# Kernel optimization log

Measured on AMD Instinct MI355X. Metric: run time of the kernel, lower is better.

The kernel has to match this reference:

```python
import jax, jax.numpy as jnp
import numpy as np

# Static graph layout: B equal-sized graphs of N nodes, DEG random edges per node.
B, N, DEG = 128, 1024, 16
F_IN, H, C = 2, 64, 2
RATIO = 0.8
E = B * N * DEG
K1 = int(np.ceil(RATIO * N))      # 820
K2 = int(np.ceil(RATIO * K1))     # 656
K3 = int(np.ceil(RATIO * K2))     # 525


def setup_inputs() -> dict:
    key = jax.random.key(0)
    ks = jax.random.split(key, 24)
    x = jax.random.normal(ks[0], (B * N, F_IN), jnp.float32)
    edge_attr = jax.random.uniform(ks[1], (E,), jnp.float32)
    # per-graph random endpoints, offset so edges stay inside each graph
    local = jax.random.randint(ks[2], (2, B, N * DEG), 0, N)
    edge_index = (local + (jnp.arange(B) * N)[None, :, None]).reshape(2, E)

    def lin(k, i, o):
        return jax.random.normal(k, (i, o), jnp.float32) / np.sqrt(i)

    def bias(k, o):
        return jax.random.normal(k, (o,), jnp.float32) * 0.01

    return {
        "x": x, "edge_attr": edge_attr,
        "W1": lin(ks[3], F_IN, H), "b1": bias(ks[4], H),
        "Wp1": lin(ks[5], H, 1), "bp1": bias(ks[6], 1),
        "W2": lin(ks[7], H, H), "b2": bias(ks[8], H),
        "Wp2": lin(ks[9], H, 1), "bp2": bias(ks[10], 1),
        "W3": lin(ks[11], H, H), "b3": bias(ks[12], H),
        "Wp3": lin(ks[13], H, 1), "bp3": bias(ks[14], 1),
        "Wl1": lin(ks[15], 2 * H, H), "bl1": bias(ks[16], H),
        "Wl2": lin(ks[17], H, H // 2), "bl2": bias(ks[18], H // 2),
        "Wl3": lin(ks[19], H // 2, C), "bl3": bias(ks[20], C),
        "edge_index": edge_index,
    }


def gcn(x, src, dst, w, W, b):
    """PyG GCNConv with gcn_norm (self-loops weight 1)."""
    h = x @ W                                       # [BN, out]
    deg = jnp.zeros((x.shape[0],), x.dtype).at[dst].add(w) + 1.0
    dinv = jax.lax.rsqrt(deg)
    norm = dinv[src] * w * dinv[dst]                # [E]
    out = jnp.zeros_like(h).at[dst].add(norm[:, None] * h[src])
    out = out + (dinv * dinv)[:, None] * h          # self-loop term
    return out + b


def sagpool(x, alive, src, dst, Wp, bp, k):
    """SAGPool: unweighted GCN scoring, per-graph top-k, x <- x * tanh(score).
    Removed nodes/edges are kept as masked (alive=False) slots -> static shapes."""
    we = (alive[src] & alive[dst]).astype(x.dtype)
    score = gcn(x, src, dst, we, Wp, bp)[:, 0]      # [BN]
    s = jnp.where(alive, score, -jnp.inf).reshape(B, N)
    _, idx = jax.lax.top_k(s, k)                    # [B, k]
    alive_new = jnp.zeros((B, N), bool).at[jnp.arange(B)[:, None], idx].set(True).reshape(-1)
    xn = jnp.where(alive_new[:, None], x * jnp.tanh(score)[:, None], 0.0)
    return xn, alive_new


def readout(x, alive):
    """concat(global_max_pool, global_mean_pool) over alive nodes per graph."""
    xr = x.reshape(B, N, -1)
    m = alive.reshape(B, N, 1)
    mx = jnp.max(jnp.where(m, xr, -jnp.inf), axis=1)
    mn = jnp.sum(jnp.where(m, xr, 0.0), axis=1) / jnp.sum(m, axis=1).astype(x.dtype)
    return jnp.concatenate([mx, mn], axis=1)        # [B, 2*H]


def _forward(x, edge_attr, W1, b1, Wp1, bp1, W2, b2, Wp2, bp2, W3, b3, Wp3, bp3,
             Wl1, bl1, Wl2, bl2, Wl3, bl3, edge_index):
    src, dst = edge_index[0], edge_index[1]
    h = jax.nn.relu(gcn(x, src, dst, edge_attr, W1, b1))
    h, a1 = sagpool(h, jnp.ones((B * N,), bool), src, dst, Wp1, bp1, K1)
    x1 = readout(h, a1)

    ea1 = edge_attr * (a1[src] & a1[dst]).astype(x.dtype)
    h = jax.nn.relu(gcn(h, src, dst, ea1, W2, b2))
    h, a2 = sagpool(h, a1, src, dst, Wp2, bp2, K2)
    x2 = readout(h, a2)

    # conv3 is called WITHOUT edge_weight -> surviving edges get weight 1
    ea2 = (a2[src] & a2[dst]).astype(x.dtype)
    h = jax.nn.relu(gcn(h, src, dst, ea2, W3, b3))
    h, a3 = sagpool(h, a2, src, dst, Wp3, bp3, K3)
    x3 = readout(h, a3)

    g = x1 + x2 + x3
    g = jax.nn.relu(g @ Wl1 + bl1)                  # dropout: eval mode (identity)
    g = jax.nn.relu(g @ Wl2 + bl2)
    return jax.nn.log_softmax(g @ Wl3 + bl3, axis=-1)


def reference(x, edge_attr, W1, b1, Wp1, bp1, W2, b2, Wp2, bp2, W3, b3, Wp3, bp3,
              Wl1, bl1, Wl2, bl2, Wl3, bl3, edge_index):
    return _forward(x, edge_attr, W1, b1, Wp1, bp1, W2, b2, Wp2, bp2, W3, b3,
                    Wp3, bp3, Wl1, bl1, Wl2, bl2, Wl3, bl3, edge_index)
```

## Files before the change

kernel.cpp:

```cpp
#include <hip/hip_runtime.h>
#include <math.h>

#define NB 128
#define NN 1024
#define BNODES (NB*NN)
#define NE 2097152
#define EPG (NE/NB)
#define EPT (EPG/NN)
#define FH 64
#define KK1 820
#define KK2 656
#define KK3 525

__global__ __launch_bounds__(1024) void k_csr(const int* __restrict__ ei,
                                              const float* __restrict__ ea,
                                              int* __restrict__ rowptr,
                                              int2* __restrict__ csr_sw,
                                              float* __restrict__ dinvW,
                                              float* __restrict__ dinvU) {
  extern __shared__ int2 lcsr[];
  __shared__ int cnt[NN];
  __shared__ int cur[NN];
  __shared__ float wsum[NN];
  int b = blockIdx.x, t = threadIdx.x;
  int node = b*NN + t;
  cnt[t] = 0;
  wsum[t] = 0.f;
  __syncthreads();
  int ebase = b*EPG;
  int se[EPT]; int de[EPT]; float we[EPT];
  #pragma unroll
  for (int i = 0; i < EPT; ++i) {
    int e = ebase + i*NN + t;
    se[i] = ei[e];
    de[i] = ei[NE + e] - b*NN;
    we[i] = ea[e];
    atomicAdd(&cnt[de[i]], 1);
    atomicAdd(&wsum[de[i]], we[i]);
  }
  __syncthreads();
  int v = cnt[t];
  for (int off = 1; off < NN; off <<= 1) {
    int u = (t >= off) ? cnt[t - off] : 0;
    __syncthreads();
    cnt[t] += u;
    __syncthreads();
  }
  int excl = cnt[t] - v;
  rowptr[node] = ebase + excl;
  cur[t] = excl;
  dinvW[node] = rsqrtf(1.f + wsum[t]);
  dinvU[node] = rsqrtf(1.f + (float)v);
  if (b == NB-1 && t == NN-1) rowptr[BNODES] = NE;
  __syncthreads();
  #pragma unroll
  for (int i = 0; i < EPT; ++i) {
    int pos = atomicAdd(&cur[de[i]], 1);
    lcsr[pos] = make_int2(se[i], __float_as_int(we[i]));
  }
  __syncthreads();
  float4* dst4 = (float4*)(csr_sw + ebase);
  const float4* src4 = (const float4*)lcsr;
  #pragma unroll
  for (int i = 0; i < EPG/2/NN; ++i)
    dst4[i*NN + t] = src4[i*NN + t];
}

template<int MODE, bool L1S>
__global__ __launch_bounds__(1024, 4) void k_gath(
    const int* __restrict__ rowptr, const int2* __restrict__ csr_sw,
    const float* __restrict__ dinvW, const float* __restrict__ src,
    const float* __restrict__ Wl,
    const float* __restrict__ bias, const float* __restrict__ Wp,
    float* __restrict__ hA, float* __restrict__ qpart) {
  extern __shared__ float sHB[];
  __shared__ float sDW[NN];
  __shared__ float sWp[32];
  __shared__ float sB[32];
  __shared__ float sW1[64];
  int b = blockIdx.x >> 1, half = blockIdx.x & 1;
  int t = threadIdx.x, l8 = t & 7;
  int gbase = b*NN;
  sDW[t] = dinvW[gbase + t];
  if (t < 32) { sWp[t] = Wp[half*32 + t]; sB[t] = bias[half*32 + t]; }
  float4* sHB4 = (float4*)sHB;
  if (L1S) {
    if (t < 32) { sW1[t] = Wl[half*32 + t]; sW1[32 + t] = Wl[64 + half*32 + t]; }
    __syncthreads();
    #pragma unroll
    for (int i = 0; i < 32; ++i) {
      int el = i*1024 + t;
      int n = el >> 5, ff = el & 31;
      float x0 = src[(size_t)(gbase + n)*2];
      float x1 = src[(size_t)(gbase + n)*2 + 1];
      sHB[n*32 + ff] = x0*sW1[ff] + x1*sW1[32 + ff];
    }
  } else {
    const float4* hB4 = (const float4*)src;
    #pragma unroll
    for (int i = 0; i < 8; ++i) {
      int idx = i*1024 + t;
      int n = idx >> 3, j = idx & 7;
      sHB4[n*8 + j] = hB4[(size_t)(gbase + n)*16 + half*8 + j];
    }
  }
  __syncthreads();
  float4 bv = ((const float4*)sB)[l8];
  float4 wp = ((const float4*)sWp)[l8];
  #pragma unroll 1
  for (int pass = 0; pass < 8; ++pass) {
    int n = pass*128 + (t >> 3);
    int gn = gbase + n;
    float dd = sDW[n];
    float4 hv = sHB4[n*8 + l8];
    float dd2 = dd*dd;
    float4 acc;
    acc.x = fmaf(dd2, hv.x, bv.x);
    acc.y = fmaf(dd2, hv.y, bv.y);
    acc.z = fmaf(dd2, hv.z, bv.z);
    acc.w = fmaf(dd2, hv.w, bv.w);
    int r0 = rowptr[gn], r1 = rowptr[gn+1];
    for (int base = r0; base < r1; base += 8) {
      int sj = 0; float cj = 0.f;
      if (base + l8 < r1) {
        int2 p = csr_sw[base + l8];
        sj = p.x - gbase;
        float w = (MODE == 2) ? 1.f : __int_as_float(p.y);
        cj = sDW[sj] * w * dd;
      }
      float4 v[8];
      #pragma unroll
      for (int j = 0; j < 8; ++j) {
        int s = __shfl(sj, j, 8);
        v[j] = sHB4[s*8 + l8];
      }
      #pragma unroll
      for (int j = 0; j < 8; ++j) {
        float c = __shfl(cj, j, 8);
        acc.x = fmaf(c, v[j].x, acc.x);
        acc.y = fmaf(c, v[j].y, acc.y);
        acc.z = fmaf(c, v[j].z, acc.z);
        acc.w = fmaf(c, v[j].w, acc.w);
      }
    }
    acc.x = fmaxf(acc.x, 0.f); acc.y = fmaxf(acc.y, 0.f);
    acc.z = fmaxf(acc.z, 0.f); acc.w = fmaxf(acc.w, 0.f);
    ((float4*)hA)[(size_t)gn*16 + half*8 + l8] = acc;
    float dot = acc.x*wp.x + acc.y*wp.y + acc.z*wp.z + acc.w*wp.w;
    dot += __shfl_xor(dot, 4, 8);
    dot += __shfl_xor(dot, 2, 8);
    dot += __shfl_xor(dot, 1, 8);
    if (l8 == 0) qpart[half*BNODES + gn] = dot;
  }
}

template<int NEXTMODE>
__global__ __launch_bounds__(1024) void k_pool(
    const int* __restrict__ rowptr, const int2* __restrict__ csr_sw,
    const float* __restrict__ qpart, const float* __restrict__ bp, int k,
    float* __restrict__ tm, int* __restrict__ aliveN,
    float* dinvW, float* dinvU) {
  __shared__ float sq[NN];
  __shared__ float sdU[NN];
  __shared__ float sc[NN];
  __shared__ float sraw[NN];
  __shared__ int ssel[NN];
  int b = blockIdx.x, t = threadIdx.x;
  int gbase = b*NN;
  float du = dinvU[gbase + t];
  sdU[t] = du;
  sq[t] = du * (qpart[gbase + t] + qpart[BNODES + gbase + t]);
  __syncthreads();
  int l16 = t & 15, g = t >> 4;
  float bpv = bp[0];
  for (int i = 0; i < 16; ++i) {
    int n = g*16 + i;
    int gn = gbase + n;
    int r0 = rowptr[gn], r1 = rowptr[gn+1];
    float sum = 0.f;
    for (int base = r0; base < r1; base += 16)
      if (base + l16 < r1) sum += sq[csr_sw[base + l16].x - gbase];
    #pragma unroll
    for (int off = 8; off; off >>= 1) sum += __shfl_xor(sum, off, 16);
    if (l16 == 0) {
      float dun = sdU[n];
      float raw = bpv + dun*(sq[n] + sum);
      sraw[n] = raw;
      sc[n] = (dun != 0.f) ? raw : -INFINITY;
    }
  }
  __syncthreads();
  float me = sc[t];
  int rank = 0;
  const float4* sc4 = (const float4*)sc;
  for (int j4 = 0; j4 < NN/4; ++j4) {
    float4 o = sc4[j4];
    int jb = j4*4;
    rank += (o.x > me) || (o.x == me && jb+0 < t);
    rank += (o.y > me) || (o.y == me && jb+1 < t);
    rank += (o.z > me) || (o.z == me && jb+2 < t);
    rank += (o.w > me) || (o.w == me && jb+3 < t);
  }
  int sel = (rank < k) ? 1 : 0;
  ssel[t] = sel;
  aliveN[gbase + t] = sel;
  tm[gbase + t] = sel ? tanhf(sraw[t]) : 0.f;
  __syncthreads();
  if (NEXTMODE != 0) {
    for (int i = 0; i < 16; ++i) {
      int n = g*16 + i;
      int gn = gbase + n;
      int r0 = rowptr[gn], r1 = rowptr[gn+1];
      float sW = 0.f, sU = 0.f;
      for (int base = r0; base < r1; base += 16)
        if (base + l16 < r1) {
          int2 p = csr_sw[base + l16];
          if (ssel[p.x - gbase]) {
            sW += (NEXTMODE == 2) ? 1.f : __int_as_float(p.y);
            sU += 1.f;
          }
        }
      #pragma unroll
      for (int off = 8; off; off >>= 1) {
        sW += __shfl_xor(sW, off, 16);
        sU += __shfl_xor(sU, off, 16);
      }
      if (l16 == 0) {
        bool dA = ssel[n] != 0;
        dinvW[gn] = dA ? rsqrtf(1.f + sW) : 0.f;
        dinvU[gn] = dA ? rsqrtf(1.f + sU) : 0.f;
      }
    }
  }
}

template<bool DOLIN>
__global__ void k_srl(const float* __restrict__ hA, const float* __restrict__ tm,
                      const int* __restrict__ aliveN, const float* __restrict__ W,
                      float* __restrict__ hB,
                      float* __restrict__ pmax, float* __restrict__ psum) {
  __shared__ float sX[64][65];
  __shared__ float sW[64*64];
  __shared__ int sAl[64];
  __shared__ float rm[4][FH], rs[4][FH];
  int t = threadIdx.x;
  int blk = blockIdx.x;
  int nb = blk*64;
  if (DOLIN)
    for (int i = t; i < 1024; i += 256) ((float4*)sW)[i] = ((const float4*)W)[i];
  if (t < 64) sAl[t] = aliveN[nb + t];
  #pragma unroll
  for (int i = 0; i < 16; ++i) {
    int gidx = (nb << 6) + i*256 + t;
    int node = gidx >> 6, f = gidx & 63;
    sX[node - nb][f] = hA[gidx] * tm[node];
  }
  __syncthreads();
  {
    int f = t & 63, r = t >> 6;
    float mx = -INFINITY, sm = 0.f;
    #pragma unroll
    for (int i = 0; i < 16; ++i) {
      int n = r + i*4;
      float v = sX[n][f];
      if (sAl[n]) { mx = fmaxf(mx, v); sm += v; }
    }
    rm[r][f] = mx; rs[r][f] = sm;
  }
  __syncthreads();
  if (t < FH) {
    float m2 = fmaxf(fmaxf(rm[0][t], rm[1][t]), fmaxf(rm[2][t], rm[3][t]));
    float s2 = rs[0][t] + rs[1][t] + rs[2][t] + rs[3][t];
    pmax[blk*FH + t] = m2;
    psum[blk*FH + t] = s2;
  }
  if (DOLIN) {
    int node = t >> 2;
    int f0 = (t & 3) * 16;
    float4 a0 = {0,0,0,0}, a1 = a0, a2 = a0, a3 = a0;
    #pragma unroll 4
    for (int k = 0; k < 64; ++k) {
      float xv = sX[node][k];
      const float4 w0 = *(const float4*)&sW[k*64 + f0];
      const float4 w1 = *(const float4*)&sW[k*64 + f0 + 4];
      const float4 w2 = *(const float4*)&sW[k*64 + f0 + 8];
      const float4 w3 = *(const float4*)&sW[k*64 + f0 + 12];
      a0.x = fmaf(xv, w0.x, a0.x); a0.y = fmaf(xv, w0.y, a0.y);
      a0.z = fmaf(xv, w0.z, a0.z); a0.w = fmaf(xv, w0.w, a0.w);
      a1.x = fmaf(xv, w1.x, a1.x); a1.y = fmaf(xv, w1.y, a1.y);
      a1.z = fmaf(xv, w1.z, a1.z); a1.w = fmaf(xv, w1.w, a1.w);
      a2.x = fmaf(xv, w2.x, a2.x); a2.y = fmaf(xv, w2.y, a2.y);
      a2.z = fmaf(xv, w2.z, a2.z); a2.w = fmaf(xv, w2.w, a2.w);
      a3.x = fmaf(xv, w3.x, a3.x); a3.y = fmaf(xv, w3.y, a3.y);
      a3.z = fmaf(xv, w3.z, a3.z); a3.w = fmaf(xv, w3.w, a3.w);
    }
    float4* dst = (float4*)(hB + (size_t)(nb + node)*FH + f0);
    dst[0] = a0; dst[1] = a1; dst[2] = a2; dst[3] = a3;
  }
}

__global__ void k_mlp(const float* __restrict__ pmax, const float* __restrict__ psum,
                      const float* __restrict__ Wl1, const float* __restrict__ bl1,
                      const float* __restrict__ Wl2, const float* __restrict__ bl2,
                      const float* __restrict__ Wl3, const float* __restrict__ bl3,
                      float* __restrict__ out) {
  __shared__ float sg[2*FH];
  __shared__ float l1[FH];
  __shared__ float l2[FH/2];
  __shared__ float l3[2];
  int b = blockIdx.x, t = threadIdx.x;
  const float kf[3] = {(float)KK1, (float)KK2, (float)KK3};
  float gm = 0.f, gs = 0.f;
  #pragma unroll
  for (int l = 0; l < 3; ++l) {
    const float* pm = pmax + (size_t)l*NB*16*FH + (b*16)*FH;
    const float* ps = psum + (size_t)l*NB*16*FH + (b*16)*FH;
    float mm = -INFINITY, ss = 0.f;
    #pragma unroll
    for (int p = 0; p < 16; ++p) {
      mm = fmaxf(mm, pm[p*FH + t]);
      ss += ps[p*FH + t];
    }
    gm += mm;
    gs += ss / kf[l];
  }
  sg[t] = gm;
  sg[FH + t] = gs;
  __syncthreads();
  float acc = bl1[t];
  #pragma unroll
  for (int k = 0; k < 2*FH; ++k) acc = fmaf(sg[k], Wl1[k*FH + t], acc);
  l1[t] = fmaxf(acc, 0.f);
  __syncthreads();
  if (t < 32) {
    float a2 = bl2[t];
    #pragma unroll
    for (int k = 0; k < FH; ++k) a2 = fmaf(l1[k], Wl2[k*32 + t], a2);
    l2[t] = fmaxf(a2, 0.f);
  }
  __syncthreads();
  if (t < 2) {
    float a3 = bl3[t];
    #pragma unroll
    for (int k = 0; k < 32; ++k) a3 = fmaf(l2[k], Wl3[k*2 + t], a3);
    l3[t] = a3;
  }
  __syncthreads();
  if (t == 0) {
    float m = fmaxf(l3[0], l3[1]);
    float lse = m + logf(expf(l3[0]-m) + expf(l3[1]-m));
    out[b*2+0] = l3[0] - lse;
    out[b*2+1] = l3[1] - lse;
  }
}

extern "C" void kernel_launch(void* const* d_in, const int* in_sizes, int n_in,
                              void* d_out, int out_size, void* d_ws, size_t ws_size,
                              hipStream_t stream) {
  const float* x   = (const float*)d_in[0];
  const float* ea  = (const float*)d_in[1];
  const float* W1  = (const float*)d_in[2];
  const float* b1  = (const float*)d_in[3];
  const float* Wp1 = (const float*)d_in[4];
  const float* bp1 = (const float*)d_in[5];
  const float* W2  = (const float*)d_in[6];
  const float* b2  = (const float*)d_in[7];
  const float* Wp2 = (const float*)d_in[8];
  const float* bp2 = (const float*)d_in[9];
  const float* W3  = (const float*)d_in[10];
  const float* b3  = (const float*)d_in[11];
  const float* Wp3 = (const float*)d_in[12];
  const float* bp3 = (const float*)d_in[13];
  const float* Wl1 = (const float*)d_in[14];
  const float* bl1 = (const float*)d_in[15];
  const float* Wl2 = (const float*)d_in[16];
  const float* bl2 = (const float*)d_in[17];
  const float* Wl3 = (const float*)d_in[18];
  const float* bl3 = (const float*)d_in[19];
  const int*   ei  = (const int*)d_in[20];
  float* out = (float*)d_out;

  int2* csr_sw = (int2*)d_ws;
  float* hA    = (float*)(csr_sw + NE);
  float* hB    = hA + (size_t)BNODES*FH;
  float* dinvW = hB + (size_t)BNODES*FH;
  float* dinvU = dinvW + BNODES;
  float* qpart = dinvU + BNODES;
  float* tm    = qpart + 2*BNODES;
  float* pmax  = tm + BNODES;
  float* psum  = pmax + 3*NB*16*FH;
  int* aliveN  = (int*)(psum + 3*NB*16*FH);
  int* rowptr  = aliveN + BNODES;

  const size_t gathLds = (size_t)NN*32*sizeof(float);
  const int gS = BNODES/64;

  k_csr<<<NB, 1024, EPG*sizeof(int2), stream>>>(ei, ea, rowptr, csr_sw, dinvW, dinvU);

  k_gath<0,true><<<NB*2, 1024, gathLds, stream>>>(rowptr, csr_sw, dinvW, x, W1, b1, Wp1, hA, qpart);
  k_pool<1><<<NB, 1024, 0, stream>>>(rowptr, csr_sw, qpart, bp1, KK1, tm, aliveN, dinvW, dinvU);
  k_srl<true><<<gS, 256, 0, stream>>>(hA, tm, aliveN, W2, hB, pmax, psum);

  k_gath<1,false><<<NB*2, 1024, gathLds, stream>>>(rowptr, csr_sw, dinvW, hB, W1, b2, Wp2, hA, qpart);
  k_pool<2><<<NB, 1024, 0, stream>>>(rowptr, csr_sw, qpart, bp2, KK2, tm, aliveN, dinvW, dinvU);
  k_srl<true><<<gS, 256, 0, stream>>>(hA, tm, aliveN, W3, hB, pmax + NB*16*FH, psum + NB*16*FH);

  k_gath<2,false><<<NB*2, 1024, gathLds, stream>>>(rowptr, csr_sw, dinvW, hB, W1, b3, Wp3, hA, qpart);
  k_pool<0><<<NB, 1024, 0, stream>>>(rowptr, csr_sw, qpart, bp3, KK3, tm, aliveN, dinvW, dinvU);
  k_srl<false><<<gS, 256, 0, stream>>>(hA, tm, aliveN, W3, hB, pmax + 2*NB*16*FH, psum + 2*NB*16*FH);

  k_mlp<<<NB, FH, 0, stream>>>(pmax, psum, Wl1, bl1, Wl2, bl2, Wl3, bl3, out);
}
```

Baseline: 445.0 us.

## Split per-graph pooling kernel into wider-grid score, top-k, and degree kernels

Replaces the monolithic per-graph k_pool (128 blocks of 1024 threads) with four kernels: q finalisation, neighbor-sum scoring, top-k ranking split four ways per graph, and degree recomputation. The aim is to spread the neighbor gathers and rank counting over far more blocks so the GPU is better occupied, instead of 128 blocks doing serial loops. In exchange it adds more kernel launches and global round trips for q and score that previously stayed in LDS. Degree recomputation now reads alive flags from global memory.

Result: faster. 375.1 us (-15.7%).

```diff
diff --git a/kernel.cpp b/kernel.cpp
--- a/kernel.cpp
+++ b/kernel.cpp
@@ -154,83 +154,86 @@
   }
 }
 
-template<int NEXTMODE>
-__global__ __launch_bounds__(1024) void k_pool(
-    const int* __restrict__ rowptr, const int2* __restrict__ csr_sw,
-    const float* __restrict__ qpart, const float* __restrict__ bp, int k,
-    float* __restrict__ tm, int* __restrict__ aliveN,
-    float* dinvW, float* dinvU) {
-  __shared__ float sq[NN];
-  __shared__ float sdU[NN];
+__global__ void k_qfin(const float* __restrict__ dinvU, const float* __restrict__ qp,
+                       float* __restrict__ q) {
+  int i = blockIdx.x*256 + threadIdx.x;
+  if (i < BNODES) q[i] = dinvU[i]*(qp[i] + qp[BNODES + i]);
+}
+
+__global__ void k_score(const int* __restrict__ rowptr, const int2* __restrict__ csr_sw,
+                        const float* __restrict__ dinvU, const float* __restrict__ q,
+                        const float* __restrict__ bp, float* __restrict__ score) {
+  int t = threadIdx.x;
+  int l16 = t & 15;
+  int d = blockIdx.x*16 + (t >> 4);
+  float du = dinvU[d];
+  float sum = 0.f;
+  if (du != 0.f) {
+    int r0 = rowptr[d], r1 = rowptr[d+1];
+    for (int base = r0; base < r1; base += 16)
+      if (base + l16 < r1) sum += q[csr_sw[base + l16].x];
+  }
+  #pragma unroll
+  for (int off = 8; off; off >>= 1) sum += __shfl_xor(sum, off, 16);
+  if (l16 == 0) score[d] = bp[0] + du*(q[d] + sum);
+}
+
+__global__ void k_topk(const float* __restrict__ score,
+                       const float* __restrict__ dinvU, int k,
+                       float* __restrict__ tm, int* __restrict__ aliveN) {
   __shared__ float sc[NN];
-  __shared__ float sraw[NN];
-  __shared__ int ssel[NN];
-  int b = blockIdx.x, t = threadIdx.x;
+  int b = blockIdx.x >> 2, p = blockIdx.x & 3;
+  int t = threadIdx.x;
   int gbase = b*NN;
-  float du = dinvU[gbase + t];
-  sdU[t] = du;
-  sq[t] = du * (qpart[gbase + t] + qpart[BNODES + gbase + t]);
-  __syncthreads();
-  int l16 = t & 15, g = t >> 4;
-  float bpv = bp[0];
-  for (int i = 0; i < 16; ++i) {
-    int n = g*16 + i;
-    int gn = gbase + n;
-    int r0 = rowptr[gn], r1 = rowptr[gn+1];
-    float sum = 0.f;
-    for (int base = r0; base < r1; base += 16)
-      if (base + l16 < r1) sum += sq[csr_sw[base + l16].x - gbase];
-    #pragma unroll
-    for (int off = 8; off; off >>= 1) sum += __shfl_xor(sum, off, 16);
-    if (l16 == 0) {
-      float dun = sdU[n];
-      float raw = bpv + dun*(sq[n] + sum);
-      sraw[n] = raw;
-      sc[n] = (dun != 0.f) ? raw : -INFINITY;
-    }
-  }
-  __syncthreads();
-  float me = sc[t];
+  #pragma unroll
+  for (int i = 0; i < 4; ++i) {
+    int n = i*256 + t;
+    sc[n] = (dinvU[gbase + n] != 0.f) ? score[gbase + n] : -INFINITY;
+  }
+  __syncthreads();
+  int n = p*256 + t;
+  int node = gbase + n;
+  float me = sc[n];
+  float raw = score[node];
   int rank = 0;
   const float4* sc4 = (const float4*)sc;
   for (int j4 = 0; j4 < NN/4; ++j4) {
     float4 o = sc4[j4];
     int jb = j4*4;
-    rank += (o.x > me) || (o.x == me && jb+0 < t);
-    rank += (o.y > me) || (o.y == me && jb+1 < t);
-    rank += (o.z > me) || (o.z == me && jb+2 < t);
-    rank += (o.w > me) || (o.w == me && jb+3 < t);
+    rank += (o.x > me) || (o.x == me && jb+0 < n);
+    rank += (o.y > me) || (o.y == me && jb+1 < n);
+    rank += (o.z > me) || (o.z == me && jb+2 < n);
+    rank += (o.w > me) || (o.w == me && jb+3 < n);
   }
   int sel = (rank < k) ? 1 : 0;
-  ssel[t] = sel;
-  aliveN[gbase + t] = sel;
-  tm[gbase + t] = sel ? tanhf(sraw[t]) : 0.f;
-  __syncthreads();
-  if (NEXTMODE != 0) {
-    for (int i = 0; i < 16; ++i) {
-      int n = g*16 + i;
-      int gn = gbase + n;
-      int r0 = rowptr[gn], r1 = rowptr[gn+1];
-      float sW = 0.f, sU = 0.f;
-      for (int base = r0; base < r1; base += 16)
-        if (base + l16 < r1) {
-          int2 p = csr_sw[base + l16];
-          if (ssel[p.x - gbase]) {
-            sW += (NEXTMODE == 2) ? 1.f : __int_as_float(p.y);
-            sU += 1.f;
-          }
-        }
-      #pragma unroll
-      for (int off = 8; off; off >>= 1) {
-        sW += __shfl_xor(sW, off, 16);
-        sU += __shfl_xor(sU, off, 16);
-      }
-      if (l16 == 0) {
-        bool dA = ssel[n] != 0;
-        dinvW[gn] = dA ? rsqrtf(1.f + sW) : 0.f;
-        dinvU[gn] = dA ? rsqrtf(1.f + sU) : 0.f;
-      }
-    }
+  aliveN[node] = sel;
+  tm[node] = sel ? tanhf(raw) : 0.f;
+}
+
+template<int MODE>
+__global__ void k_degs(const int* __restrict__ rowptr, const int2* __restrict__ csr_sw,
+                       const int* __restrict__ alive,
+                       float* __restrict__ dinvW, float* __restrict__ dinvU) {
+  int t = threadIdx.x;
+  int l16 = t & 15;
+  int d = blockIdx.x*16 + (t >> 4);
+  int r0 = rowptr[d], r1 = rowptr[d+1];
+  float sW = 0.f, sU = 0.f;
+  for (int base = r0; base < r1; base += 16) {
+    if (base + l16 < r1) {
+      int2 p = csr_sw[base + l16];
+      if (alive[p.x]) { sW += (MODE == 2) ? 1.f : __int_as_float(p.y); sU += 1.f; }
+    }
+  }
+  #pragma unroll
+  for (int off = 8; off; off >>= 1) {
+    sW += __shfl_xor(sW, off, 16);
+    sU += __shfl_xor(sU, off, 16);
+  }
+  if (l16 == 0) {
+    bool dA = (alive[d] != 0);
+    dinvW[d] = dA ? rsqrtf(1.f + sW) : 0.f;
+    dinvU[d] = dA ? rsqrtf(1.f + sU) : 0.f;
   }
 }
 
@@ -386,7 +389,9 @@
   float* dinvW = hB + (size_t)BNODES*FH;
   float* dinvU = dinvW + BNODES;
   float* qpart = dinvU + BNODES;
-  float* tm    = qpart + 2*BNODES;
+  float* q     = qpart + 2*BNODES;
+  float* score = q + BNODES;
+  float* tm    = score + BNODES;
   float* pmax  = tm + BNODES;
   float* psum  = pmax + 3*NB*16*FH;
   int* aliveN  = (int*)(psum + 3*NB*16*FH);
@@ -394,19 +399,29 @@
 
   const size_t gathLds = (size_t)NN*32*sizeof(float);
   const int gS = BNODES/64;
+  const int gG = BNODES/16;
+  const int gN = BNODES/256;
 
   k_csr<<<NB, 1024, EPG*sizeof(int2), stream>>>(ei, ea, rowptr, csr_sw, dinvW, dinvU);
 
   k_gath<0,true><<<NB*2, 1024, gathLds, stream>>>(rowptr, csr_sw, dinvW, x, W1, b1, Wp1, hA, qpart);
-  k_pool<1><<<NB, 1024, 0, stream>>>(rowptr, csr_sw, qpart, bp1, KK1, tm, aliveN, dinvW, dinvU);
+  k_qfin<<<gN, 256, 0, stream>>>(dinvU, qpart, q);
+  k_score<<<gG, 256, 0, stream>>>(rowptr, csr_sw, dinvU, q, bp1, score);
+  k_topk<<<NB*4, 256, 0, stream>>>(score, dinvU, KK1, tm, aliveN);
   k_srl<true><<<gS, 256, 0, stream>>>(hA, tm, aliveN, W2, hB, pmax, psum);
+  k_degs<1><<<gG, 256, 0, stream>>>(rowptr, csr_sw, aliveN, dinvW, dinvU);
 
   k_gath<1,false><<<NB*2, 1024, gathLds, stream>>>(rowptr, csr_sw, dinvW, hB, W1, b2, Wp2, hA, qpart);
-  k_pool<2><<<NB, 1024, 0, stream>>>(rowptr, csr_sw, qpart, bp2, KK2, tm, aliveN, dinvW, dinvU);
+  k_qfin<<<gN, 256, 0, stream>>>(dinvU, qpart, q);
+  k_score<<<gG, 256, 0, stream>>>(rowptr, csr_sw, dinvU, q, bp2, score);
+  k_topk<<<NB*4, 256, 0, stream>>>(score, dinvU, KK2, tm, aliveN);
   k_srl<true><<<gS, 256, 0, stream>>>(hA, tm, aliveN, W3, hB, pmax + NB*16*FH, psum + NB*16*FH);
+  k_degs<2><<<gG, 256, 0, stream>>>(rowptr, csr_sw, aliveN, dinvW, dinvU);
 
   k_gath<2,false><<<NB*2, 1024, gathLds, stream>>>(rowptr, csr_sw, dinvW, hB, W1, b3, Wp3, hA, qpart);
-  k_pool<0><<<NB, 1024, 0, stream>>>(rowptr, csr_sw, qpart, bp3, KK3, tm, aliveN, dinvW, dinvU);
+  k_qfin<<<gN, 256, 0, stream>>>(dinvU, qpart, q);
+  k_score<<<gG, 256, 0, stream>>>(rowptr, csr_sw, dinvU, q, bp3, score);
+  k_topk<<<NB*4, 256, 0, stream>>>(score, dinvU, KK3, tm, aliveN);
   k_srl<false><<<gS, 256, 0, stream>>>(hA, tm, aliveN, W3, hB, pmax + 2*NB*16*FH, psum + 2*NB*16*FH);
 
   k_mlp<<<NB, FH, 0, stream>>>(pmax, psum, Wl1, bl1, Wl2, bl2, Wl3, bl3, out);
```
